# Performance work log

Measured on AMD Instinct MI355X. Metric: run time of the kernel, lower is better.

## Reference

```python
import math
import jax, jax.numpy as jnp
import numpy as np

B, T, D, FF, E = 32, 1024, 512, 2048, 8
CAPACITY_FACTOR = 1.25
CAP = int(math.ceil(CAPACITY_FACTOR * B * T / E))  # per-expert capacity (5120)


def setup_inputs() -> dict:
    key = jax.random.key(0)
    ks = jax.random.split(key, 18)
    s = 0.02
    inp = {
        "x": jax.random.normal(ks[0], (B, T, D), dtype=jnp.float32),
        # routers (linear heads, std=0.02, zero bias)
        "Wr_sp": jax.random.normal(ks[1], (D, E)) * s,
        "br_sp": jnp.zeros((E,), jnp.float32),
        "Wr_fq": jax.random.normal(ks[2], (D, E)) * s,
        "br_fq": jnp.zeros((E,), jnp.float32),
        # shared dense FFN
        "Ws1": jax.random.normal(ks[3], (D, FF)) * s,
        "bs1": jnp.zeros((FF,), jnp.float32),
        "Ws2": jax.random.normal(ks[4], (FF, D)) * s,
        "bs2": jnp.zeros((D,), jnp.float32),
        # spatial specialist bank (E experts)
        "W1_sp": jax.random.normal(ks[5], (E, D, FF)) * s,
        "b1_sp": jnp.zeros((E, FF), jnp.float32),
        "W2_sp": jax.random.normal(ks[6], (E, FF, D)) * s,
        "b2_sp": jnp.zeros((E, D), jnp.float32),
        # spectral specialist bank (E experts)
        "W1_fq": jax.random.normal(ks[7], (E, D, FF)) * s,
        "b1_fq": jnp.zeros((E, FF), jnp.float32),
        "W2_fq": jax.random.normal(ks[8], (E, FF, D)) * s,
        "b2_fq": jnp.zeros((E, D), jnp.float32),
    }
    return inp


def _bank_residual(x2, Wr, br, W1, b1, W2, b2):
    """Top-1 capacity-routed expert bank residual. x2: [N, D]."""
    N, d = x2.shape
    e = Wr.shape[1]
    logits = x2 @ Wr + br                                  # [N, E]
    probs = jax.nn.softmax(logits, axis=-1)
    expert = jnp.argmax(probs, axis=-1)                    # [N] top-1
    gate = jnp.take_along_axis(probs, expert[:, None], axis=-1)[:, 0]
    oneh = jax.nn.one_hot(expert, e, dtype=x2.dtype)       # [N, E]
    # position of each token within its expert's queue (0-based)
    pos = (jnp.cumsum(oneh, axis=0) * oneh).sum(-1).astype(jnp.int32) - 1
    keep = pos < CAP                                       # fallback-to-shared when saturated
    slot = expert.astype(jnp.int32) * CAP + jnp.minimum(pos, CAP - 1)
    xd = jnp.where(keep[:, None], x2, 0.0)
    buf = jnp.zeros((e * CAP, d), x2.dtype).at[slot].add(xd)  # dispatch (dropped tokens add 0)
    buf = buf.reshape(e, CAP, d)
    h = jax.nn.gelu(jnp.einsum('ecd,edf->ecf', buf, W1) + b1[:, None, :], approximate=False)
    out = jnp.einsum('ecf,efd->ecd', h, W2) + b2[:, None, :]
    y = out.reshape(e * CAP, d)[slot]                      # combine (gather back)
    return y * (gate * keep.astype(x2.dtype))[:, None]


def reference(x, Wr_sp, br_sp, Wr_fq, br_fq, Ws1, bs1, Ws2, bs2,
              W1_sp, b1_sp, W2_sp, b2_sp, W1_fq, b1_fq, W2_fq, b2_fq):
    b, t, d = x.shape
    x2 = x.reshape(b * t, d)
    shared = jax.nn.gelu(x2 @ Ws1 + bs1, approximate=False) @ Ws2 + bs2
    y = shared
    y = y + _bank_residual(x2, Wr_sp, br_sp, W1_sp, b1_sp, W2_sp, b2_sp)
    y = y + _bank_residual(x2, Wr_fq, br_fq, W1_fq, b1_fq, W2_fq, b2_fq)
    return y.reshape(b, t, d)
```

## Files before the change

kernel.cpp:

```cpp
#include <hip/hip_runtime.h>
#include <hip/hip_bf16.h>
#include <math.h>

#define N_TOK 32768
#define DIMD  512
#define FFD   2048
#define NE    8
#define CAPQ  5120
#define TPE   40
#define NBLK  128

typedef __attribute__((ext_vector_type(8))) short          bf16x8;
typedef __attribute__((ext_vector_type(4))) float          f32x4;
typedef __attribute__((ext_vector_type(8))) unsigned short u16x8;

__device__ __forceinline__ unsigned short f2bf(float f) {
  union { float f; unsigned u; } v; v.f = f;
  unsigned r = v.u + 0x7fffu + ((v.u >> 16) & 1u);
  return (unsigned short)(r >> 16);
}

__device__ __forceinline__ float gelu_f(float v) {
  float t = v * v;
  float q = fmaf(-0.0713548162f, t, -1.5957691216f);
  float w = v * q;
  float d = 1.0f + __expf(w);
  return v * __builtin_amdgcn_rcpf(d);
}

#define GLL16(gsrc, ldst)                                                      \
  __builtin_amdgcn_global_load_lds(                                            \
      (const __attribute__((address_space(1))) void*)(gsrc),                   \
      (__attribute__((address_space(3))) void*)(ldst), 16, 0, 0)

__global__ __launch_bounds__(256) void transpose_cvt3_kernel(
    const float* __restrict__ s0, const float* __restrict__ s1,
    const float* __restrict__ s2,
    unsigned short* __restrict__ d0, unsigned short* __restrict__ d1,
    unsigned short* __restrict__ d2, int R, int C) {
  __shared__ unsigned short tile[32][33];
  const int z = blockIdx.z;
  const float* in; unsigned short* out;
  if (z == 0)      { in = s0;                            out = d0; }
  else if (z <= 8) { in = s1 + (size_t)(z - 1) * R * C;  out = d1 + (size_t)(z - 1) * R * C; }
  else             { in = s2 + (size_t)(z - 9) * R * C;  out = d2 + (size_t)(z - 9) * R * C; }
  int c0 = blockIdx.x * 32, r0 = blockIdx.y * 32;
  int tx = threadIdx.x & 31, ty = threadIdx.x >> 5;
  #pragma unroll
  for (int i = 0; i < 4; i++) {
    int r = ty + i * 8;
    tile[r][tx] = f2bf(in[(size_t)(r0 + r) * C + c0 + tx]);
  }
  __syncthreads();
  #pragma unroll
  for (int i = 0; i < 4; i++) {
    int c = ty + i * 8;
    out[(size_t)(c0 + c) * R + r0 + tx] = tile[tx][c];
  }
}

__global__ __launch_bounds__(256) void router_kernel(
    const float* __restrict__ x, unsigned short* __restrict__ xb,
    const float* __restrict__ WrS, const float* __restrict__ brS,
    const float* __restrict__ WrF, const float* __restrict__ brF,
    int* __restrict__ expS, float* __restrict__ gateS,
    int* __restrict__ expF, float* __restrict__ gateF) {
  __shared__ float wS[DIMD * NE], wF[DIMD * NE];
  for (int i = threadIdx.x; i < DIMD * NE / 4; i += 256) {
    ((float4*)wS)[i] = ((const float4*)WrS)[i];
    ((float4*)wF)[i] = ((const float4*)WrF)[i];
  }
  __syncthreads();
  const int w = threadIdx.x >> 6, lane = threadIdx.x & 63;
  const int n0 = (blockIdx.x * 4 + w) * 8;
  for (int t = 0; t < 8; t++) {
    const int n = n0 + t;
    const float* xr = x + (size_t)n * DIMD + lane * 8;
    float4 xa = *(const float4*)xr, xb4 = *(const float4*)(xr + 4);
    float xv[8] = {xa.x, xa.y, xa.z, xa.w, xb4.x, xb4.y, xb4.z, xb4.w};
    u16x8 xo;
    #pragma unroll
    for (int j = 0; j < 8; j++) xo[j] = f2bf(xv[j]);
    *(u16x8*)(xb + (size_t)n * DIMD + lane * 8) = xo;
    float aS[NE], aF[NE];
    #pragma unroll
    for (int e = 0; e < NE; e++) { aS[e] = 0.f; aF[e] = 0.f; }
    #pragma unroll
    for (int j = 0; j < 8; j++) {
      const int k = lane * 8 + j;
      const float* ps = &wS[k * NE];
      const float* pf = &wF[k * NE];
      #pragma unroll
      for (int e = 0; e < NE; e++) { aS[e] += xv[j] * ps[e]; aF[e] += xv[j] * pf[e]; }
    }
    #pragma unroll
    for (int e = 0; e < NE; e++)
      for (int off = 32; off; off >>= 1) {
        aS[e] += __shfl_xor(aS[e], off);
        aF[e] += __shfl_xor(aF[e], off);
      }
    if (lane == 0) {
      float l[NE];
      #pragma unroll
      for (int e = 0; e < NE; e++) l[e] = aS[e] + brS[e];
      float m = l[0]; int am = 0;
      #pragma unroll
      for (int e = 1; e < NE; e++) if (l[e] > m) { m = l[e]; am = e; }
      float s = 0.f;
      #pragma unroll
      for (int e = 0; e < NE; e++) s += __expf(l[e] - m);
      expS[n] = am; gateS[n] = __builtin_amdgcn_rcpf(s);
      #pragma unroll
      for (int e = 0; e < NE; e++) l[e] = aF[e] + brF[e];
      m = l[0]; am = 0;
      #pragma unroll
      for (int e = 1; e < NE; e++) if (l[e] > m) { m = l[e]; am = e; }
      s = 0.f;
      #pragma unroll
      for (int e = 0; e < NE; e++) s += __expf(l[e] - m);
      expF[n] = am; gateF[n] = __builtin_amdgcn_rcpf(s);
    }
  }
}

__global__ __launch_bounds__(256) void scan_count_kernel(
    const int* __restrict__ expS, const int* __restrict__ expF,
    int* __restrict__ blockcnt) {
  const int b = blockIdx.x, t = threadIdx.x;
  const int w = t >> 6, lane = t & 63;
  const int eS_ = expS[b * 256 + t], eF_ = expF[b * 256 + t];
  __shared__ int cnt[2][4][NE];
  #pragma unroll
  for (int q = 0; q < NE; q++) {
    unsigned long long mS = __ballot(eS_ == q);
    unsigned long long mF = __ballot(eF_ == q);
    if (lane == 0) { cnt[0][w][q] = __popcll(mS); cnt[1][w][q] = __popcll(mF); }
  }
  __syncthreads();
  if (t < 16) {
    const int bank = t >> 3, q = t & 7;
    blockcnt[bank * NBLK * NE + b * NE + q] =
        cnt[bank][0][q] + cnt[bank][1][q] + cnt[bank][2][q] + cnt[bank][3][q];
  }
}

__global__ __launch_bounds__(64) void scan_base_kernel(
    const int* __restrict__ blockcnt, int* __restrict__ blockbase,
    int* __restrict__ meta) {
  __shared__ int tot[2][NE];
  const int t = threadIdx.x;
  if (t < 16) {
    const int bank = t >> 3, q = t & 7;
    int run = 0;
    for (int i = 0; i < NBLK; i++) {
      int v = blockcnt[bank * NBLK * NE + i * NE + q];
      blockbase[bank * NBLK * NE + i * NE + q] = run;
      run += v;
    }
    tot[bank][q] = run;
  }
  __syncthreads();
  if (t == 0) {
    int hb_ = 0;
    for (int q = 0; q < NE; q++) {
      int cc = tot[0][q]; if (cc > CAPQ) cc = CAPQ;
      meta[q] = cc; meta[NE + q] = hb_;
      hb_ += ((cc + 127) >> 7) << 7;
    }
    hb_ = 0;
    for (int q = 0; q < NE; q++) {
      int cc = tot[1][q]; if (cc > CAPQ) cc = CAPQ;
      meta[2 * NE + q] = cc; meta[3 * NE + q] = hb_;
      hb_ += ((cc + 127) >> 7) << 7;
    }
  }
}

__global__ __launch_bounds__(256) void scan_write_kernel(
    const int* __restrict__ expS, const int* __restrict__ expF,
    const int* __restrict__ blockbase,
    int* __restrict__ idxS, int* __restrict__ idxF) {
  const int b = blockIdx.x, t = threadIdx.x;
  const int w = t >> 6, lane = t & 63;
  const int n = b * 256 + t;
  const int eS_ = expS[n], eF_ = expF[n];
  __shared__ int wcnt[2][4][NE];
  const unsigned long long ltmask = ((unsigned long long)1 << lane) - 1;
  int rS = 0, rF = 0;
  #pragma unroll
  for (int q = 0; q < NE; q++) {
    unsigned long long mS = __ballot(eS_ == q);
    unsigned long long mF = __ballot(eF_ == q);
    if (eS_ == q) rS = __popcll(mS & ltmask);
    if (eF_ == q) rF = __popcll(mF & ltmask);
    if (lane == 0) { wcnt[0][w][q] = __popcll(mS); wcnt[1][w][q] = __popcll(mF); }
  }
  __syncthreads();
  int pS = blockbase[0 * NBLK * NE + b * NE + eS_] + rS;
  int pF = blockbase[1 * NBLK * NE + b * NE + eF_] + rF;
  #pragma unroll
  for (int wv = 0; wv < 4; wv++) {
    if (wv < w) { pS += wcnt[0][wv][eS_]; pF += wcnt[1][wv][eF_]; }
  }
  if (pS < CAPQ) idxS[eS_ * CAPQ + pS] = n;
  if (pF < CAPQ) idxF[eF_ * CAPQ + pF] = n;
}

template <int EPI, bool GATHER, bool BANKED>
__global__ __launch_bounds__(512, 4) void gemm_kernel(
    const unsigned short* __restrict__ A,
    const unsigned short* __restrict__ Bt,
    const float* __restrict__ bias,
    const int* __restrict__ idx, const int* __restrict__ cnt,
    const int* __restrict__ hb, const float* __restrict__ gate,
    unsigned short* __restrict__ hidOut, float* __restrict__ fOut) {
  constexpr int K  = (EPI == 0) ? DIMD : FFD;
  constexpr int NC = (EPI == 0) ? FFD : DIMD;
  constexpr int NT = K / 64;

  __shared__ __align__(16) unsigned short lA[2][128 * 64];
  __shared__ __align__(16) unsigned short lB[2][128 * 64];

  const int tid = threadIdx.x;
  const int w = tid >> 6, lane = tid & 63;

  const int gx = gridDim.x;
  const int nwg = gx * gridDim.y;
  int flat = blockIdx.y * gx + blockIdx.x;
  {
    const int q8 = nwg >> 3, r8 = nwg & 7;
    const int xcd = flat & 7, loc = flat >> 3;
    flat = (xcd < r8 ? xcd * (q8 + 1) : r8 * (q8 + 1) + (xcd - r8) * q8) + loc;
  }
  const int bx = flat % gx, by = flat / gx;

  int e = 0, r0, cnte = 0;
  if (BANKED) {
    e = by / TPE;
    r0 = (by - e * TPE) * 128;
    cnte = cnt[e];
    if (r0 >= cnte) return;
  } else {
    r0 = by * 128;
  }

  const int srow = lane >> 3;
  const int sch  = (lane & 7) ^ srow;
  const unsigned short* aP[2];
  const unsigned short* bP[2];
  const size_t bcol0 = (size_t)(BANKED ? e * NC : 0) + (size_t)bx * 128;
  #pragma unroll
  for (int i = 0; i < 2; i++) {
    const int ri = (i * 8 + w) * 8 + srow;
    size_t arow;
    if (GATHER) {
      int s = r0 + ri;
      int tok = (s < cnte) ? idx[e * CAPQ + s] : 0;
      arow = (size_t)tok;
    } else if (BANKED) {
      arow = (size_t)(hb[e] + r0 + ri);
    } else {
      arow = (size_t)(r0 + ri);
    }
    aP[i] = A + arow * K + sch * 8;
    bP[i] = Bt + (bcol0 + ri) * K + sch * 8;
  }

  f32x4 acc[2][4];
  #pragma unroll
  for (int m = 0; m < 2; m++)
    #pragma unroll
    for (int n = 0; n < 4; n++) acc[m][n] = (f32x4){0.f, 0.f, 0.f, 0.f};

  const int wr = w >> 1, wc = w & 1;
  const int grp = lane >> 4, l15 = lane & 15;
  const int swz = l15 & 7;
  int aoff[2], boff[4], kche[2];
  #pragma unroll
  for (int m = 0; m < 2; m++) aoff[m] = (wr * 32 + m * 16 + l15) * 64;
  #pragma unroll
  for (int n = 0; n < 4; n++) boff[n] = (wc * 64 + n * 16 + l15) * 64;
  #pragma unroll
  for (int kk = 0; kk < 2; kk++) kche[kk] = ((kk * 4 + grp) ^ swz) * 8;

  auto stage = [&](int buf, int k0) {
    char* la = (char*)&lA[buf][0] + (unsigned)w * 1024;
    char* lb = (char*)&lB[buf][0] + (unsigned)w * 1024;
    #pragma unroll
    for (int i = 0; i < 2; i++) {
      GLL16(aP[i] + k0, la + i * 8192);
      GLL16(bP[i] + k0, lb + i * 8192);
    }
  };

  stage(0, 0);
  int cur = 0;
  #pragma unroll 1
  for (int t = 0; t < NT; t++) {
    if (t + 1 < NT) {
      stage(cur ^ 1, (t + 1) * 64);
      asm volatile("s_waitcnt vmcnt(4)" ::: "memory");
    } else {
      asm volatile("s_waitcnt vmcnt(0)" ::: "memory");
    }
    __builtin_amdgcn_s_barrier();
    __builtin_amdgcn_sched_barrier(0);
    const unsigned short* A_ = &lA[cur][0];
    const unsigned short* B_ = &lB[cur][0];
    #pragma unroll
    for (int kk = 0; kk < 2; kk++) {
      const int co = kche[kk];
      bf16x8 af[2], bfv[4];
      #pragma unroll
      for (int m = 0; m < 2; m++) af[m] = *(const bf16x8*)&A_[aoff[m] + co];
      #pragma unroll
      for (int n = 0; n < 4; n++) bfv[n] = *(const bf16x8*)&B_[boff[n] + co];
      __builtin_amdgcn_s_setprio(1);
      #pragma unroll
      for (int m = 0; m < 2; m++)
        #pragma unroll
        for (int n = 0; n < 4; n++)
          acc[m][n] = __builtin_amdgcn_mfma_f32_16x16x32_bf16(af[m], bfv[n], acc[m][n], 0, 0, 0);
      __builtin_amdgcn_s_setprio(0);
    }
    __builtin_amdgcn_sched_barrier(0);
    __builtin_amdgcn_s_barrier();
    cur ^= 1;
  }

  const int grp4 = grp * 4;
  if constexpr (EPI == 0) {
    const size_t hrow0 = (size_t)((BANKED ? hb[e] : 0) + r0);
    const float* bP2 = bias + (BANKED ? e * NC : 0) + bx * 128;
    #pragma unroll
    for (int m = 0; m < 2; m++)
      #pragma unroll
      for (int j = 0; j < 4; j++) {
        const int rloc = wr * 32 + m * 16 + grp4 + j;
        unsigned short* hrow = hidOut + (hrow0 + rloc) * FFD + bx * 128;
        #pragma unroll
        for (int n = 0; n < 4; n++) {
          const int cloc = wc * 64 + n * 16 + l15;
          float v = acc[m][n][j] + bP2[cloc];
          hrow[cloc] = f2bf(gelu_f(v));
        }
      }
  } else if constexpr (EPI == 1) {
    const float* bP2 = bias + bx * 128;
    #pragma unroll
    for (int m = 0; m < 2; m++)
      #pragma unroll
      for (int j = 0; j < 4; j++) {
        const int rloc = wr * 32 + m * 16 + grp4 + j;
        float* orow = fOut + (size_t)(r0 + rloc) * DIMD + bx * 128;
        #pragma unroll
        for (int n = 0; n < 4; n++) {
          const int cloc = wc * 64 + n * 16 + l15;
          orow[cloc] = acc[m][n][j] + bP2[cloc];
        }
      }
  } else {
    const float* bP2 = bias + e * NC + bx * 128;
    const int* idxe = idx + e * CAPQ + r0;
    #pragma unroll
    for (int m = 0; m < 2; m++)
      #pragma unroll
      for (int j = 0; j < 4; j++) {
        const int rloc = wr * 32 + m * 16 + grp4 + j;
        if (r0 + rloc < cnte) {
          const int tok = idxe[rloc];
          const float gv = gate[tok];
          float* orow = fOut + (size_t)tok * DIMD + bx * 128;
          #pragma unroll
          for (int n = 0; n < 4; n++) {
            const int cloc = wc * 64 + n * 16 + l15;
            orow[cloc] += (acc[m][n][j] + bP2[cloc]) * gv;
          }
        }
      }
  }
}

extern "C" void kernel_launch(void* const* d_in, const int* in_sizes, int n_in,
                              void* d_out, int out_size, void* d_ws, size_t ws_size,
                              hipStream_t stream) {
  const float* x   = (const float*)d_in[0];
  const float* WrS = (const float*)d_in[1];
  const float* brS = (const float*)d_in[2];
  const float* WrF = (const float*)d_in[3];
  const float* brF = (const float*)d_in[4];
  const float* Ws1 = (const float*)d_in[5];
  const float* bs1 = (const float*)d_in[6];
  const float* Ws2 = (const float*)d_in[7];
  const float* bs2 = (const float*)d_in[8];
  const float* W1s = (const float*)d_in[9];
  const float* b1s = (const float*)d_in[10];
  const float* W2s = (const float*)d_in[11];
  const float* b2s = (const float*)d_in[12];
  const float* W1f = (const float*)d_in[13];
  const float* b1f = (const float*)d_in[14];
  const float* W2f = (const float*)d_in[15];
  const float* b2f = (const float*)d_in[16];
  float* out = (float*)d_out;

  char* ws = (char*)d_ws;
  size_t off = 0;
  auto alloc = [&](size_t b) { char* p = ws + off; off += (b + 255) & ~(size_t)255; return p; };
  unsigned short* xb     = (unsigned short*)alloc((size_t)N_TOK * DIMD * 2);
  unsigned short* ws1t   = (unsigned short*)alloc((size_t)FFD * DIMD * 2);
  unsigned short* ws2t   = (unsigned short*)alloc((size_t)DIMD * FFD * 2);
  unsigned short* w1st   = (unsigned short*)alloc((size_t)NE * FFD * DIMD * 2);
  unsigned short* w2st   = (unsigned short*)alloc((size_t)NE * DIMD * FFD * 2);
  unsigned short* w1ft   = (unsigned short*)alloc((size_t)NE * FFD * DIMD * 2);
  unsigned short* w2ft   = (unsigned short*)alloc((size_t)NE * DIMD * FFD * 2);
  unsigned short* hidden = (unsigned short*)alloc((size_t)(N_TOK + NE * 128) * FFD * 2);
  int*   expS = (int*)alloc((size_t)N_TOK * 4);
  int*   expF = (int*)alloc((size_t)N_TOK * 4);
  float* gS   = (float*)alloc((size_t)N_TOK * 4);
  float* gF   = (float*)alloc((size_t)N_TOK * 4);
  int*   idxS = (int*)alloc((size_t)NE * CAPQ * 4);
  int*   idxF = (int*)alloc((size_t)NE * CAPQ * 4);
  int*   meta = (int*)alloc(4 * NE * 4);
  int*   blockcnt  = (int*)alloc((size_t)2 * NBLK * NE * 4);
  int*   blockbase = (int*)alloc((size_t)2 * NBLK * NE * 4);
  if (off > ws_size) return;

  int* cntS = meta;           int* hbS = meta + NE;
  int* cntF = meta + 2 * NE;  int* hbF = meta + 3 * NE;

  transpose_cvt3_kernel<<<dim3(FFD / 32, DIMD / 32, 17), 256, 0, stream>>>(
      Ws1, W1s, W1f, ws1t, w1st, w1ft, DIMD, FFD);
  transpose_cvt3_kernel<<<dim3(DIMD / 32, FFD / 32, 17), 256, 0, stream>>>(
      Ws2, W2s, W2f, ws2t, w2st, w2ft, FFD, DIMD);
  router_kernel<<<N_TOK / 32, 256, 0, stream>>>(x, xb, WrS, brS, WrF, brF, expS, gS, expF, gF);
  scan_count_kernel<<<NBLK, 256, 0, stream>>>(expS, expF, blockcnt);
  scan_base_kernel<<<1, 64, 0, stream>>>(blockcnt, blockbase, meta);
  scan_write_kernel<<<NBLK, 256, 0, stream>>>(expS, expF, blockbase, idxS, idxF);

  gemm_kernel<0, false, false><<<dim3(FFD / 128, N_TOK / 128), 512, 0, stream>>>(
      xb, ws1t, bs1, nullptr, nullptr, nullptr, nullptr, hidden, nullptr);
  gemm_kernel<1, false, false><<<dim3(DIMD / 128, N_TOK / 128), 512, 0, stream>>>(
      hidden, ws2t, bs2, nullptr, nullptr, nullptr, nullptr, nullptr, out);
  gemm_kernel<0, true, true><<<dim3(FFD / 128, NE * TPE), 512, 0, stream>>>(
      xb, w1st, b1s, idxS, cntS, hbS, nullptr, hidden, nullptr);
  gemm_kernel<2, false, true><<<dim3(DIMD / 128, NE * TPE), 512, 0, stream>>>(
      hidden, w2st, b2s, idxS, cntS, hbS, gS, nullptr, out);
  gemm_kernel<0, true, true><<<dim3(FFD / 128, NE * TPE), 512, 0, stream>>>(
      xb, w1ft, b1f, idxF, cntF, hbF, nullptr, hidden, nullptr);
  gemm_kernel<2, false, true><<<dim3(DIMD / 128, NE * TPE), 512, 0, stream>>>(
      hidden, w2ft, b2f, idxF, cntF, hbF, gF, nullptr, out);
}
```

Before: 784.7 us.

## Batch shared and expert FFN1 GEMMs into one z-indexed launch

Adds a gemm_ffn1z kernel that uses blockIdx.z to pick between the shared FFN1 and the two expert-bank FFN1 GEMMs, so they run in a single launch. Each writes its hidden activations to a separate region, and the FFN2 launches follow. The aim is to fill the GPU better and drop launch gaps and tail effects from the small, partly empty banked grids. It needs a larger workspace for the hidden buffers and falls back to fewer-merged tiers when the workspace is too small. Separately, the GEMM main loop is factored into a shared helper.

```diff
diff --git a/kernel.cpp b/kernel.cpp
--- a/kernel.cpp
+++ b/kernel.cpp
@@ -9,6 +9,7 @@
 #define CAPQ  5120
 #define TPE   40
 #define NBLK  128
+#define HROWS_BANK (N_TOK + NE * 128)
 
 typedef __attribute__((ext_vector_type(8))) short          bf16x8;
 typedef __attribute__((ext_vector_type(4))) float          f32x4;
@@ -206,6 +207,82 @@
   if (pF < CAPQ) idxF[eF_ * CAPQ + pF] = n;
 }
 
+struct GemmCtx {
+  const unsigned short* aSrc0;
+  const unsigned short* aSrc1;
+  const unsigned short* bSrc0;
+  const unsigned short* bSrc1;
+};
+
+template <int K>
+__device__ __forceinline__ void gemm_core(
+    const GemmCtx& cx, unsigned short (*lA)[128 * 64], unsigned short (*lB)[128 * 64],
+    int w, int lane, f32x4 (&acc)[2][4],
+    int wr, int wc, int grp, int l15) {
+  constexpr int NT = K / 64;
+  const int swz = l15 & 7;
+  int aoff[2], boff[4], kche[2];
+  #pragma unroll
+  for (int m = 0; m < 2; m++) aoff[m] = (wr * 32 + m * 16 + l15) * 64;
+  #pragma unroll
+  for (int n = 0; n < 4; n++) boff[n] = (wc * 64 + n * 16 + l15) * 64;
+  #pragma unroll
+  for (int kk = 0; kk < 2; kk++) kche[kk] = ((kk * 4 + grp) ^ swz) * 8;
+
+  auto stage = [&](int buf, int k0) {
+    char* la = (char*)&lA[buf][0] + (unsigned)w * 1024;
+    char* lb = (char*)&lB[buf][0] + (unsigned)w * 1024;
+    GLL16(cx.aSrc0 + k0, la);
+    GLL16(cx.aSrc1 + k0, la + 8192);
+    GLL16(cx.bSrc0 + k0, lb);
+    GLL16(cx.bSrc1 + k0, lb + 8192);
+  };
+
+  stage(0, 0);
+  int cur = 0;
+  #pragma unroll 1
+  for (int t = 0; t < NT; t++) {
+    if (t + 1 < NT) {
+      stage(cur ^ 1, (t + 1) * 64);
+      asm volatile("s_waitcnt vmcnt(4)" ::: "memory");
+    } else {
+      asm volatile("s_waitcnt vmcnt(0)" ::: "memory");
+    }
+    __builtin_amdgcn_s_barrier();
+    __builtin_amdgcn_sched_barrier(0);
+    const unsigned short* A_ = &lA[cur][0];
+    const unsigned short* B_ = &lB[cur][0];
+    #pragma unroll
+    for (int kk = 0; kk < 2; kk++) {
+      const int co = kche[kk];
+      bf16x8 af[2], bfv[4];
+      #pragma unroll
+      for (int m = 0; m < 2; m++) af[m] = *(const bf16x8*)&A_[aoff[m] + co];
+      #pragma unroll
+      for (int n = 0; n < 4; n++) bfv[n] = *(const bf16x8*)&B_[boff[n] + co];
+      __builtin_amdgcn_s_setprio(1);
+      #pragma unroll
+      for (int m = 0; m < 2; m++)
+        #pragma unroll
+        for (int n = 0; n < 4; n++)
+          acc[m][n] = __builtin_amdgcn_mfma_f32_16x16x32_bf16(af[m], bfv[n], acc[m][n], 0, 0, 0);
+      __builtin_amdgcn_s_setprio(0);
+    }
+    __builtin_amdgcn_sched_barrier(0);
+    __builtin_amdgcn_s_barrier();
+    cur ^= 1;
+  }
+}
+
+__device__ __forceinline__ void xcd_swizzle(int gx, int gy, int& bx, int& by) {
+  const int nwg = gx * gy;
+  int flat = by * gx + bx;
+  const int q8 = nwg >> 3, r8 = nwg & 7;
+  const int xcd = flat & 7, loc = flat >> 3;
+  flat = (xcd < r8 ? xcd * (q8 + 1) : r8 * (q8 + 1) + (xcd - r8) * q8) + loc;
+  bx = flat % gx; by = flat / gx;
+}
+
 template <int EPI, bool GATHER, bool BANKED>
 __global__ __launch_bounds__(512, 4) void gemm_kernel(
     const unsigned short* __restrict__ A,
@@ -216,23 +293,14 @@
     unsigned short* __restrict__ hidOut, float* __restrict__ fOut) {
   constexpr int K  = (EPI == 0) ? DIMD : FFD;
   constexpr int NC = (EPI == 0) ? FFD : DIMD;
-  constexpr int NT = K / 64;
 
   __shared__ __align__(16) unsigned short lA[2][128 * 64];
   __shared__ __align__(16) unsigned short lB[2][128 * 64];
 
   const int tid = threadIdx.x;
   const int w = tid >> 6, lane = tid & 63;
-
-  const int gx = gridDim.x;
-  const int nwg = gx * gridDim.y;
-  int flat = blockIdx.y * gx + blockIdx.x;
-  {
-    const int q8 = nwg >> 3, r8 = nwg & 7;
-    const int xcd = flat & 7, loc = flat >> 3;
-    flat = (xcd < r8 ? xcd * (q8 + 1) : r8 * (q8 + 1) + (xcd - r8) * q8) + loc;
-  }
-  const int bx = flat % gx, by = flat / gx;
+  int bx = blockIdx.x, by = blockIdx.y;
+  xcd_swizzle(gridDim.x, gridDim.y, bx, by);
 
   int e = 0, r0, cnte = 0;
   if (BANKED) {
@@ -246,24 +314,27 @@
 
   const int srow = lane >> 3;
   const int sch  = (lane & 7) ^ srow;
-  const unsigned short* aP[2];
-  const unsigned short* bP[2];
   const size_t bcol0 = (size_t)(BANKED ? e * NC : 0) + (size_t)bx * 128;
-  #pragma unroll
-  for (int i = 0; i < 2; i++) {
-    const int ri = (i * 8 + w) * 8 + srow;
-    size_t arow;
+  GemmCtx cx;
+  {
+    const int ri0 = (0 * 8 + w) * 8 + srow;
+    const int ri1 = (1 * 8 + w) * 8 + srow;
+    size_t ar0, ar1;
     if (GATHER) {
-      int s = r0 + ri;
-      int tok = (s < cnte) ? idx[e * CAPQ + s] : 0;
-      arow = (size_t)tok;
+      int s0 = r0 + ri0, s1 = r0 + ri1;
+      ar0 = (size_t)((s0 < cnte) ? idx[e * CAPQ + s0] : 0);
+      ar1 = (size_t)((s1 < cnte) ? idx[e * CAPQ + s1] : 0);
     } else if (BANKED) {
-      arow = (size_t)(hb[e] + r0 + ri);
+      ar0 = (size_t)(hb[e] + r0 + ri0);
+      ar1 = (size_t)(hb[e] + r0 + ri1);
     } else {
-      arow = (size_t)(r0 + ri);
-    }
-    aP[i] = A + arow * K + sch * 8;
-    bP[i] = Bt + (bcol0 + ri) * K + sch * 8;
+      ar0 = (size_t)(r0 + ri0);
+      ar1 = (size_t)(r0 + ri1);
+    }
+    cx.aSrc0 = A + ar0 * K + sch * 8;
+    cx.aSrc1 = A + ar1 * K + sch * 8;
+    cx.bSrc0 = Bt + (bcol0 + ri0) * K + sch * 8;
+    cx.bSrc1 = Bt + (bcol0 + ri1) * K + sch * 8;
   }
 
   f32x4 acc[2][4];
@@ -274,59 +345,7 @@
 
   const int wr = w >> 1, wc = w & 1;
   const int grp = lane >> 4, l15 = lane & 15;
-  const int swz = l15 & 7;
-  int aoff[2], boff[4], kche[2];
-  #pragma unroll
-  for (int m = 0; m < 2; m++) aoff[m] = (wr * 32 + m * 16 + l15) * 64;
-  #pragma unroll
-  for (int n = 0; n < 4; n++) boff[n] = (wc * 64 + n * 16 + l15) * 64;
-  #pragma unroll
-  for (int kk = 0; kk < 2; kk++) kche[kk] = ((kk * 4 + grp) ^ swz) * 8;
-
-  auto stage = [&](int buf, int k0) {
-    char* la = (char*)&lA[buf][0] + (unsigned)w * 1024;
-    char* lb = (char*)&lB[buf][0] + (unsigned)w * 1024;
-    #pragma unroll
-    for (int i = 0; i < 2; i++) {
-      GLL16(aP[i] + k0, la + i * 8192);
-      GLL16(bP[i] + k0, lb + i * 8192);
-    }
-  };
-
-  stage(0, 0);
-  int cur = 0;
-  #pragma unroll 1
-  for (int t = 0; t < NT; t++) {
-    if (t + 1 < NT) {
-      stage(cur ^ 1, (t + 1) * 64);
-      asm volatile("s_waitcnt vmcnt(4)" ::: "memory");
-    } else {
-      asm volatile("s_waitcnt vmcnt(0)" ::: "memory");
-    }
-    __builtin_amdgcn_s_barrier();
-    __builtin_amdgcn_sched_barrier(0);
-    const unsigned short* A_ = &lA[cur][0];
-    const unsigned short* B_ = &lB[cur][0];
-    #pragma unroll
-    for (int kk = 0; kk < 2; kk++) {
-      const int co = kche[kk];
-      bf16x8 af[2], bfv[4];
-      #pragma unroll
-      for (int m = 0; m < 2; m++) af[m] = *(const bf16x8*)&A_[aoff[m] + co];
-      #pragma unroll
-      for (int n = 0; n < 4; n++) bfv[n] = *(const bf16x8*)&B_[boff[n] + co];
-      __builtin_amdgcn_s_setprio(1);
-      #pragma unroll
-      for (int m = 0; m < 2; m++)
-        #pragma unroll
-        for (int n = 0; n < 4; n++)
-          acc[m][n] = __builtin_amdgcn_mfma_f32_16x16x32_bf16(af[m], bfv[n], acc[m][n], 0, 0, 0);
-      __builtin_amdgcn_s_setprio(0);
-    }
-    __builtin_amdgcn_sched_barrier(0);
-    __builtin_amdgcn_s_barrier();
-    cur ^= 1;
-  }
+  gemm_core<K>(cx, lA, lB, w, lane, acc, wr, wc, grp, l15);
 
   const int grp4 = grp * 4;
   if constexpr (EPI == 0) {
@@ -379,6 +398,103 @@
         }
       }
   }
+}
+
+__global__ __launch_bounds__(512, 4) void gemm_ffn1z(
+    const unsigned short* __restrict__ xb,
+    const unsigned short* __restrict__ ws1t,
+    const unsigned short* __restrict__ w1st,
+    const unsigned short* __restrict__ w1ft,
+    const float* __restrict__ bs1, const float* __restrict__ b1s,
+    const float* __restrict__ b1f,
+    const int* __restrict__ idxS, const int* __restrict__ cntS,
+    const int* __restrict__ hbS,
+    const int* __restrict__ idxF, const int* __restrict__ cntF,
+    const int* __restrict__ hbF,
+    unsigned short* __restrict__ hid,
+    long long hb1, long long hb2, int zoff) {
+  constexpr int K = DIMD, NC = FFD;
+
+  __shared__ __align__(16) unsigned short lA[2][128 * 64];
+  __shared__ __align__(16) unsigned short lB[2][128 * 64];
+
+  const int tid = threadIdx.x;
+  const int w = tid >> 6, lane = tid & 63;
+  const int z = (int)blockIdx.z + zoff;
+
+  const unsigned short* Bt;
+  const float* bias;
+  const int *idx = nullptr, *cnt = nullptr, *hb = nullptr;
+  long long hidbase;
+  bool banked;
+  if (z == 0)      { Bt = ws1t; bias = bs1; hidbase = 0;   banked = false; }
+  else if (z == 1) { Bt = w1st; bias = b1s; idx = idxS; cnt = cntS; hb = hbS;
+                     hidbase = hb1; banked = true; }
+  else             { Bt = w1ft; bias = b1f; idx = idxF; cnt = cntF; hb = hbF;
+                     hidbase = hb2; banked = true; }
+
+  int bx = blockIdx.x, by = blockIdx.y;
+  xcd_swizzle(gridDim.x, gridDim.y, bx, by);
+
+  int e = 0, r0, cnte = 0;
+  if (banked) {
+    e = by / TPE;
+    r0 = (by - e * TPE) * 128;
+    cnte = cnt[e];
+    if (r0 >= cnte) return;
+  } else {
+    if (by >= N_TOK / 128) return;
+    r0 = by * 128;
+  }
+
+  const int srow = lane >> 3;
+  const int sch  = (lane & 7) ^ srow;
+  const size_t bcol0 = (size_t)(banked ? e * NC : 0) + (size_t)bx * 128;
+  GemmCtx cx;
+  {
+    const int ri0 = (0 * 8 + w) * 8 + srow;
+    const int ri1 = (1 * 8 + w) * 8 + srow;
+    size_t ar0, ar1;
+    if (banked) {
+      int s0 = r0 + ri0, s1 = r0 + ri1;
+      ar0 = (size_t)((s0 < cnte) ? idx[e * CAPQ + s0] : 0);
+      ar1 = (size_t)((s1 < cnte) ? idx[e * CAPQ + s1] : 0);
+    } else {
+      ar0 = (size_t)(r0 + ri0);
+      ar1 = (size_t)(r0 + ri1);
+    }
+    cx.aSrc0 = xb + ar0 * K + sch * 8;
+    cx.aSrc1 = xb + ar1 * K + sch * 8;
+    cx.bSrc0 = Bt + (bcol0 + ri0) * K + sch * 8;
+    cx.bSrc1 = Bt + (bcol0 + ri1) * K + sch * 8;
+  }
+
+  f32x4 acc[2][4];
+  #pragma unroll
+  for (int m = 0; m < 2; m++)
+    #pragma unroll
+    for (int n = 0; n < 4; n++) acc[m][n] = (f32x4){0.f, 0.f, 0.f, 0.f};
+
+  const int wr = w >> 1, wc = w & 1;
+  const int grp = lane >> 4, l15 = lane & 15;
+  gemm_core<K>(cx, lA, lB, w, lane, acc, wr, wc, grp, l15);
+
+  const int grp4 = grp * 4;
+  const size_t hrow0 = (size_t)(hidbase + (banked ? hb[e] : 0) + r0);
+  const float* bP2 = bias + (banked ? e * NC : 0) + bx * 128;
+  #pragma unroll
+  for (int m = 0; m < 2; m++)
+    #pragma unroll
+    for (int j = 0; j < 4; j++) {
+      const int rloc = wr * 32 + m * 16 + grp4 + j;
+      unsigned short* hrow = hid + (hrow0 + rloc) * FFD + bx * 128;
+      #pragma unroll
+      for (int n = 0; n < 4; n++) {
+        const int cloc = wc * 64 + n * 16 + l15;
+        float v = acc[m][n][j] + bP2[cloc];
+        hrow[cloc] = f2bf(gelu_f(v));
+      }
+    }
 }
 
 extern "C" void kernel_launch(void* const* d_in, const int* in_sizes, int n_in,
@@ -413,7 +529,6 @@
   unsigned short* w2st   = (unsigned short*)alloc((size_t)NE * DIMD * FFD * 2);
   unsigned short* w1ft   = (unsigned short*)alloc((size_t)NE * FFD * DIMD * 2);
   unsigned short* w2ft   = (unsigned short*)alloc((size_t)NE * DIMD * FFD * 2);
-  unsigned short* hidden = (unsigned short*)alloc((size_t)(N_TOK + NE * 128) * FFD * 2);
   int*   expS = (int*)alloc((size_t)N_TOK * 4);
   int*   expF = (int*)alloc((size_t)N_TOK * 4);
   float* gS   = (float*)alloc((size_t)N_TOK * 4);
@@ -423,7 +538,13 @@
   int*   meta = (int*)alloc(4 * NE * 4);
   int*   blockcnt  = (int*)alloc((size_t)2 * NBLK * NE * 4);
   int*   blockbase = (int*)alloc((size_t)2 * NBLK * NE * 4);
-  if (off > ws_size) return;
+  unsigned short* hidden = (unsigned short*)(ws + off);
+  const size_t remain = (ws_size > off) ? ws_size - off : 0;
+  const size_t bytes3 = (size_t)(N_TOK + 2 * HROWS_BANK) * FFD * 2;
+  const size_t bytes2 = (size_t)(2 * HROWS_BANK) * FFD * 2;
+  const size_t bytes1 = (size_t)HROWS_BANK * FFD * 2;
+  const int tier = (remain >= bytes3) ? 3 : (remain >= bytes2) ? 2 : 1;
+  if (remain < bytes1) return;
 
   int* cntS = meta;           int* hbS = meta + NE;
   int* cntF = meta + 2 * NE;  int* hbF = meta + 3 * NE;
@@ -437,16 +558,45 @@
   scan_base_kernel<<<1, 64, 0, stream>>>(blockcnt, blockbase, meta);
   scan_write_kernel<<<NBLK, 256, 0, stream>>>(expS, expF, blockbase, idxS, idxF);
 
-  gemm_kernel<0, false, false><<<dim3(FFD / 128, N_TOK / 128), 512, 0, stream>>>(
-      xb, ws1t, bs1, nullptr, nullptr, nullptr, nullptr, hidden, nullptr);
-  gemm_kernel<1, false, false><<<dim3(DIMD / 128, N_TOK / 128), 512, 0, stream>>>(
-      hidden, ws2t, bs2, nullptr, nullptr, nullptr, nullptr, nullptr, out);
-  gemm_kernel<0, true, true><<<dim3(FFD / 128, NE * TPE), 512, 0, stream>>>(
-      xb, w1st, b1s, idxS, cntS, hbS, nullptr, hidden, nullptr);
-  gemm_kernel<2, false, true><<<dim3(DIMD / 128, NE * TPE), 512, 0, stream>>>(
-      hidden, w2st, b2s, idxS, cntS, hbS, gS, nullptr, out);
-  gemm_kernel<0, true, true><<<dim3(FFD / 128, NE * TPE), 512, 0, stream>>>(
-      xb, w1ft, b1f, idxF, cntF, hbF, nullptr, hidden, nullptr);
-  gemm_kernel<2, false, true><<<dim3(DIMD / 128, NE * TPE), 512, 0, stream>>>(
-      hidden, w2ft, b2f, idxF, cntF, hbF, gF, nullptr, out);
-}
+  const dim3 gFFN2sh(DIMD / 128, N_TOK / 128);
+  const dim3 gFFN2bk(DIMD / 128, NE * TPE);
+
+  if (tier == 3) {
+    const long long hb1 = N_TOK, hb2 = N_TOK + HROWS_BANK;
+    gemm_ffn1z<<<dim3(FFD / 128, NE * TPE, 3), 512, 0, stream>>>(
+        xb, ws1t, w1st, w1ft, bs1, b1s, b1f,
+        idxS, cntS, hbS, idxF, cntF, hbF, hidden, hb1, hb2, 0);
+    gemm_kernel<1, false, false><<<gFFN2sh, 512, 0, stream>>>(
+        hidden, ws2t, bs2, nullptr, nullptr, nullptr, nullptr, nullptr, out);
+    gemm_kernel<2, false, true><<<gFFN2bk, 512, 0, stream>>>(
+        hidden + (size_t)hb1 * FFD, w2st, b2s, idxS, cntS, hbS, gS, nullptr, out);
+    gemm_kernel<2, false, true><<<gFFN2bk, 512, 0, stream>>>(
+        hidden + (size_t)hb2 * FFD, w2ft, b2f, idxF, cntF, hbF, gF, nullptr, out);
+  } else if (tier == 2) {
+    gemm_kernel<0, false, false><<<dim3(FFD / 128, N_TOK / 128), 512, 0, stream>>>(
+        xb, ws1t, bs1, nullptr, nullptr, nullptr, nullptr, hidden, nullptr);
+    gemm_kernel<1, false, false><<<gFFN2sh, 512, 0, stream>>>(
+        hidden, ws2t, bs2, nullptr, nullptr, nullptr, nullptr, nullptr, out);
+    const long long hb1 = 0, hb2 = HROWS_BANK;
+    gemm_ffn1z<<<dim3(FFD / 128, NE * TPE, 2), 512, 0, stream>>>(
+        xb, ws1t, w1st, w1ft, bs1, b1s, b1f,
+        idxS, cntS, hbS, idxF, cntF, hbF, hidden, hb1, hb2, 1);
+    gemm_kernel<2, false, true><<<gFFN2bk, 512, 0, stream>>>(
+        hidden, w2st, b2s, idxS, cntS, hbS, gS, nullptr, out);
+    gemm_kernel<2, false, true><<<gFFN2bk, 512, 0, stream>>>(
+        hidden + (size_t)hb2 * FFD, w2ft, b2f, idxF, cntF, hbF, gF, nullptr, out);
+  } else {
+    gemm_kernel<0, false, false><<<dim3(FFD / 128, N_TOK / 128), 512, 0, stream>>>(
+        xb, ws1t, bs1, nullptr, nullptr, nullptr, nullptr, hidden, nullptr);
+    gemm_kernel<1, false, false><<<gFFN2sh, 512, 0, stream>>>(
+        hidden, ws2t, bs2, nullptr, nullptr, nullptr, nullptr, nullptr, out);
+    gemm_kernel<0, true, true><<<dim3(FFD / 128, NE * TPE), 512, 0, stream>>>(
+        xb, w1st, b1s, idxS, cntS, hbS, nullptr, hidden, nullptr);
+    gemm_kernel<2, false, true><<<gFFN2bk, 512, 0, stream>>>(
+        hidden, w2st, b2s, idxS, cntS, hbS, gS, nullptr, out);
+    gemm_kernel<0, true, true><<<dim3(FFD / 128, NE * TPE), 512, 0, stream>>>(
+        xb, w1ft, b1f, idxF, cntF, hbF, nullptr, hidden, nullptr);
+    gemm_kernel<2, false, true><<<gFFN2bk, 512, 0, stream>>>(
+        hidden, w2ft, b2f, idxF, cntF, hbF, gF, nullptr, out);
+  }
+}
```

After: 786.7 us. Within noise of the previous version (+0.3%).
